# Optimization experiments

Measured on AMD Instinct MI355X. Metric: run time of the kernel, lower is better.

## Reference

```python
import jax, jax.numpy as jnp
import numpy as np

B, FI, FO, K, DIM_STYLE, H, W = 8, 512, 512, 3, 512, 64, 64
EPS = 1e-8


def setup_inputs() -> dict:
    key = jax.random.key(0)
    ks = jax.random.split(key, 5)
    return {
        "x": jax.random.normal(ks[0], (B, FI, H, W), dtype=jnp.float32),
        "style": jax.random.normal(ks[1], (B, DIM_STYLE), dtype=jnp.float32),
        "w": jax.random.normal(ks[2], (FO, FI, K, K), dtype=jnp.float32),
        "mod_w": jax.random.normal(ks[3], (FI, DIM_STYLE), dtype=jnp.float32),
        "mod_b": jax.random.normal(ks[4], (FI,), dtype=jnp.float32),
    }


def _fir_filter(dtype):
    # upfirdn2d.setup_filter([1,3,3,1]): normalize 1D to sum 1, outer product -> 4x4, sum 1
    f1 = jnp.array([1.0, 3.0, 3.0, 1.0], dtype=dtype)
    f1 = f1 / jnp.sum(f1)
    f = jnp.outer(f1, f1)
    # gain = up**2 = 4 applied inside upfirdn2d; filter is symmetric so flip is a no-op
    return (f * 4.0)[::-1, ::-1]


def _mod_conv_up(x, style, w, mod_w, mod_b):
    # modLinear: F.linear(style, mod_w * dim_style**-0.5, bias=mod_b)
    s = style @ (mod_w * (DIM_STYLE ** -0.5)).T + mod_b  # [B, FI]
    # modulate: w_scale * style broadcast over input channels
    w_scale = (FI * K * K) ** -0.5
    wm = w[None] * (w_scale * s[:, None, :, None, None])  # [B, FO, FI, K, K]
    # demodulate
    demod = jax.lax.rsqrt(jnp.sum(wm * wm, axis=(2, 3, 4)) + EPS)  # [B, FO]
    wm = wm * demod[:, :, None, None, None]
    # conv2d_resample up=2 fast path == conv_transpose2d(stride=2, padding=0) per sample,
    def tconv(xs, ws):  # xs [FI,H,W], ws [FO,FI,K,K]
        y = jax.lax.conv_general_dilated(
            xs[None], ws[:, :, ::-1, ::-1],
            window_strides=(1, 1), padding=[(K - 1, K - 1), (K - 1, K - 1)],
            lhs_dilation=(2, 2),
            dimension_numbers=("NCHW", "OIHW", "NCHW"))
        return y[0]

    y = jax.vmap(tconv)(x, wm)  # [B, FO, 2H+1, 2W+1]
    # FIR low-pass: upfirdn2d(pad=[1,1,1,1], gain=4) -> output [B, FO, 2H, 2W]
    f = _fir_filter(y.dtype)
    Bn, C, Hh, Ww = y.shape
    yf = y.reshape(Bn * C, 1, Hh, Ww)
    yf = jax.lax.conv_general_dilated(
        yf, f[None, None], window_strides=(1, 1), padding=[(1, 1), (1, 1)],
        dimension_numbers=("NCHW", "OIHW", "NCHW"))
    return yf.reshape(Bn, C, Hh - 1, Ww - 1)


def reference(x, style, w, mod_w, mod_b):
    return _mod_conv_up(x, style, w, mod_w, mod_b)
```

## Files before the change

kernel.cpp:

```cpp
#include <hip/hip_runtime.h>

typedef _Float16 f16;
typedef f16 f16x8 __attribute__((ext_vector_type(8)));
typedef float f32x4 __attribute__((ext_vector_type(4)));

#define OFF_SMOD  0u
#define OFF_SSQ   16384u
#define OFF_DEMOD 32768u
#define OFF_WSQ   49152u
#define OFF_WPAR  1097728u
#define OFF_XP    5816320u
#define XP_BYTES  35685376u
#define OFF_YP    41501696u
#define WS_NEED   190792704u
#define PLANE     4556

__global__ void style_kernel(const float* __restrict__ style, const float* __restrict__ mod_w,
                             const float* __restrict__ mod_b, float* __restrict__ smod,
                             float* __restrict__ ssq) {
    int b = blockIdx.x;
    int fi = threadIdx.x;
    __shared__ float st[512];
    st[fi] = style[b * 512 + fi];
    __syncthreads();
    float sum = 0.f;
    const float* mw = mod_w + (size_t)fi * 512;
    for (int d = 0; d < 512; ++d) sum += st[d] * mw[d];
    float s = sum * 0.04419417382415922f  + mod_b[fi];
    smod[b * 512 + fi] = s * 0.014731391274719741f ;
    ssq[b * 512 + fi] = s * s;
}

__global__ void wsq_kernel(const float* __restrict__ w, float* __restrict__ wsq) {
    int fo = blockIdx.x;
    int fi = threadIdx.x;
    const float* p = w + ((size_t)fo * 512 + fi) * 9;
    float s = 0.f;
#pragma unroll
    for (int k = 0; k < 9; ++k) { float v = p[k]; s += v * v; }
    wsq[fo * 512 + fi] = s;
}

__global__ void demod_kernel(const float* __restrict__ ssq, const float* __restrict__ wsq,
                             float* __restrict__ demod) {
    int b = blockIdx.x >> 1;
    int fo = (blockIdx.x & 1) * 256 + threadIdx.x;
    __shared__ float sq[512];
    for (int i = threadIdx.x; i < 512; i += 256) sq[i] = ssq[b * 512 + i];
    __syncthreads();
    float sum = 0.f;
    const float* wr = wsq + (size_t)fo * 512;
    for (int fi = 0; fi < 512; ++fi) sum += sq[fi] * wr[fi];
    demod[b * 512 + fo] = rsqrtf(sum * (1.0f / 4608.0f) + 1e-8f);
}

__global__ void xp_kernel(const float* __restrict__ x, const float* __restrict__ smod,
                          f16* __restrict__ xp) {
    int id = blockIdx.x;
    int fc = id & 7;
    int h = (id >> 3) & 63;
    int b = id >> 9;
    int fi0 = fc * 64;
    __shared__ f16 tile[64 * 65];
    int tid = threadIdx.x;
#pragma unroll
    for (int it = 0; it < 16; ++it) {
        int e = it * 256 + tid;
        int i = e >> 6, wc = e & 63;
        float v = x[(((size_t)(b * 512 + fi0 + i)) * 64 + h) * 64 + wc];
        tile[i * 65 + wc] = (f16)(v * smod[b * 512 + fi0 + i]);
    }
    __syncthreads();
#pragma unroll
    for (int it = 0; it < 16; ++it) {
        int e = it * 256 + tid;
        int wc = e >> 6, i = e & 63;
        xp[((size_t)(b * 4356 + (h + 1) * 66 + (wc + 1))) * 512 + fi0 + i] = tile[i * 65 + wc];
    }
}

__global__ void wpar2_kernel(const float* __restrict__ w, f16* __restrict__ wpar2) {
    const int wi_[9] = {8, 6, 2, 0, 7, 1, 5, 3, 4};
    int fo = blockIdx.x;
#pragma unroll
    for (int half = 0; half < 2; ++half) {
        int fi = half * 256 + threadIdx.x;
        const float* p = w + ((size_t)fo * 512 + fi) * 9;
        int fc = fi >> 5, ch = fi & 31;
#pragma unroll
        for (int s = 0; s < 9; ++s)
            wpar2[(((size_t)s * 16 + fc) * 512 + fo) * 32 + ch] = (f16)p[wi_[s]];
    }
}

__global__ void ring2_kernel(f16* __restrict__ P) {
    int idx = blockIdx.x * 256 + threadIdx.x;
    if (idx >= 16384 * 133) return;
    int slab = idx / 133, r = idx - slab * 133;
    f16* base = P + (size_t)slab * PLANE;
    if (r < 68) base[r] = (f16)0.f;
    else base[(r - 67) * 68] = (f16)0.f;
}

template <int C>
__device__ __forceinline__ void tconv_body(const f16* __restrict__ wpar2, const f16* __restrict__ xp,
                                           f16* __restrict__ P, f16* Xs, int b, int fg, int n0t) {
    constexpr int NT   = (C == 0) ? 4 : (C == 3) ? 1 : 2;
    constexpr int SB   = (C == 0) ? 0 : (C == 1) ? 4 : (C == 2) ? 6 : 8;
    constexpr int LB   = (C <= 1) ? 67 : (C == 2) ? 1 : 0;
    constexpr int WOFF = (C <= 1) ? 0 : (C == 2) ? 66 : 67;
    constexpr int WLEN = (C <= 1) ? 195 : (C == 2) ? 129 : 128;
    constexpr int CH4  = WLEN * 4;
    constexpr int offs[4] = {(C == 0) ? -67 : (C == 1) ? -66 : (C == 2) ? -1 : 0,
                             (C == 0) ? -66 : 0, -1, 0};

    int tid = threadIdx.x, lane = tid & 63, wave = tid >> 6;
    int wm = wave >> 1, wn = wave & 1, kb = lane >> 4, lr = lane & 15;
    int n0 = n0t << 7, fo0 = fg << 7;
    int WB = b * 4356 + n0 + WOFF;
    int bmax = b * 4356 + 4356;

    f32x4 acc[4][4];
#pragma unroll
    for (int m = 0; m < 4; ++m)
#pragma unroll
        for (int n = 0; n < 4; ++n) acc[m][n] = (f32x4){0.f, 0.f, 0.f, 0.f};

    int4 xr[4];
    f16x8 afA[4], afB[4];

    const f16* abase = wpar2 + ((size_t)(fo0 + wm * 64 + lr)) * 32 + (size_t)kb * 8;
    auto loadA = [&](int q, f16x8* dst) {
        int fc = q / NT, tap = q - fc * NT;
        const f16* p = abase + (size_t)((SB + tap) * 16 + fc) * (512 * 32);
#pragma unroll
        for (int m = 0; m < 4; ++m) dst[m] = *(const f16x8*)(p + m * 16 * 32);
    };
    auto loadX = [&](int k) {
        int fi0 = k * 32;
#pragma unroll
        for (int it = 0; it < 4; ++it) {
            int idx = it * 256 + tid;
            int4 v = {0, 0, 0, 0};
            if (idx < CH4) {
                int r = idx >> 2, part = idx & 3;
                int pr = WB + r;
                if (pr <= bmax) v = *(const int4*)(xp + ((size_t)pr * 512 + fi0 + part * 8));
            }
            xr[it] = v;
        }
    };
    auto writeX = [&]() {
#pragma unroll
        for (int it = 0; it < 4; ++it) {
            int idx = it * 256 + tid;
            if (idx < CH4) {
                int r = idx >> 2, part = idx & 3;
                *(int4*)((char*)Xs + ((((r * 4 + part) ^ (r & 7)) << 4))) = xr[it];
            }
        }
    };

    loadA(0, afA);
    loadX(0);
    for (int k = 0; k < 16; ++k) {
        __syncthreads();
        writeX();
        __syncthreads();
        if (k < 15) loadX(k + 1);
#pragma unroll
        for (int tap = 0; tap < NT; ++tap) {
            int q = k * NT + tap;
            if (q + 1 < 16 * NT) loadA(q + 1, afB);
            f16x8 bf[4];
#pragma unroll
            for (int n = 0; n < 4; ++n) {
                int r = wn * 64 + n * 16 + lr + offs[tap] + LB;
                bf[n] = *(const f16x8*)((char*)Xs + ((((r * 4 + kb) ^ (r & 7)) << 4)));
            }
            __builtin_amdgcn_s_setprio(1);
#pragma unroll
            for (int m = 0; m < 4; ++m)
#pragma unroll
                for (int n = 0; n < 4; ++n)
                    acc[m][n] = __builtin_amdgcn_mfma_f32_16x16x32_f16(afA[m], bf[n], acc[m][n], 0, 0, 0);
            __builtin_amdgcn_s_setprio(0);
#pragma unroll
            for (int m = 0; m < 4; ++m) afA[m] = afB[m];
        }
    }
    size_t slab = (size_t)(C * 8 + b) * 512;
#pragma unroll
    for (int m = 0; m < 4; ++m) {
#pragma unroll
        for (int j = 0; j < 4; ++j) {
            int fo = fo0 + wm * 64 + m * 16 + kb * 4 + j;
            f16* pb = P + (slab + fo) * PLANE;
#pragma unroll
            for (int n = 0; n < 4; ++n) {
                int nn = n0 + wn * 64 + n * 16 + lr;
                int t = (nn * 993) >> 16;
                int s = nn - t * 66;
                pb[(t + 1) * 68 + (s + 1)] = (f16)acc[m][n][j];
            }
        }
    }
}

__global__ __launch_bounds__(256, 3) void tconv2_kernel(const f16* __restrict__ wpar2,
                                                        const f16* __restrict__ xp,
                                                        f16* __restrict__ P) {
    __shared__ __align__(16) f16 Xs[780 * 8];
    int id = blockIdx.x;
    int b = id & 7;
    int r = id >> 3;
    int c = r / 136;
    int r2 = r - c * 136;
    int fg = r2 / 34;
    int n0t = r2 - fg * 34;
    switch (c) {
        case 0: tconv_body<0>(wpar2, xp, P, Xs, b, fg, n0t); break;
        case 1: tconv_body<1>(wpar2, xp, P, Xs, b, fg, n0t); break;
        case 2: tconv_body<2>(wpar2, xp, P, Xs, b, fg, n0t); break;
        default: tconv_body<3>(wpar2, xp, P, Xs, b, fg, n0t); break;
    }
}

__global__ __launch_bounds__(256) void fir2_kernel(const f16* __restrict__ P,
                                                   const float* __restrict__ demod,
                                                   float* __restrict__ out) {
    int bid = blockIdx.x;
    int rc = bid & 7;
    int fo = (bid >> 3) & 511;
    int b = bid >> 12;
    int OY0 = rc * 16;

    __shared__ f16 yr[19][2][72];
    int tid = threadIdx.x;
#pragma unroll
    for (int it = 0; it < 3; ++it) {
        int ci = it * 256 + tid;
        if (ci < 646) {
            int rr = ci / 34, rem = ci - rr * 34;
            int pxx = rem / 17, ck = rem - pxx * 17;
            int oy = OY0 - 1 + rr;
            int pyy = oy & 1, t = oy >> 1;
            const f16* src = P + ((size_t)((pyy * 2 + pxx) * 8 + b) * 512 + fo) * PLANE
                               + (t + 1) * 68 + ck * 4;
            *(int2*)&yr[rr][pxx][ck * 4] = *(const int2*)src;
        }
    }
    __syncthreads();
    float dm = demod[b * 512 + fo];
    int OX = tid & 127, rg = tid >> 7;
    const float f4[4] = {0.25f, 0.75f, 0.75f, 0.25f};
    float hrow[11];
#pragma unroll
    for (int r = 0; r < 11; ++r) {
        int rr = rg * 8 + r;
        float h = 0.f;
#pragma unroll
        for (int bb = 0; bb < 4; ++bb) {
            int ox = OX - 1 + bb;
            h += f4[bb] * (float)yr[rr][ox & 1][(ox >> 1) + 1];
        }
        hrow[r] = h;
    }
    size_t ob = ((size_t)(b * 512 + fo)) * 128 * 128 + (size_t)OY0 * 128 + OX;
#pragma unroll
    for (int i = 0; i < 8; ++i) {
        float a = f4[0] * hrow[i] + f4[1] * hrow[i + 1] + f4[2] * hrow[i + 2] + f4[3] * hrow[i + 3];
        out[ob + (size_t)(rg * 8 + i) * 128] = a * dm;
    }
}

extern "C" void kernel_launch(void* const* d_in, const int* in_sizes, int n_in,
                              void* d_out, int out_size, void* d_ws, size_t ws_size,
                              hipStream_t stream) {
    const float* x = (const float*)d_in[0];
    const float* style = (const float*)d_in[1];
    const float* w = (const float*)d_in[2];
    const float* mod_w = (const float*)d_in[3];
    const float* mod_b = (const float*)d_in[4];
    float* out = (float*)d_out;

    char* ws = (char*)d_ws;
    float* smod = (float*)(ws + OFF_SMOD);
    float* ssq = (float*)(ws + OFF_SSQ);
    float* demod = (float*)(ws + OFF_DEMOD);
    float* wsq = (float*)(ws + OFF_WSQ);
    f16* wpar2 = (f16*)(ws + OFF_WPAR);
    f16* xp = (f16*)(ws + OFF_XP);
    f16* P = (f16*)(ws + OFF_YP);

    style_kernel<<<8, 512, 0, stream>>>(style, mod_w, mod_b, smod, ssq);
    wsq_kernel<<<512, 512, 0, stream>>>(w, wsq);
    demod_kernel<<<16, 256, 0, stream>>>(ssq, wsq, demod);
    wpar2_kernel<<<512, 256, 0, stream>>>(w, wpar2);
    hipMemsetAsync(xp, 0, XP_BYTES, stream);
    xp_kernel<<<4096, 256, 0, stream>>>(x, smod, xp);
    ring2_kernel<<<8512, 256, 0, stream>>>(P);
    tconv2_kernel<<<4352, 256, 0, stream>>>(wpar2, xp, P);
    fir2_kernel<<<32768, 256, 0, stream>>>(P, demod, out);
}
```

Measured before the change: 401.4 us.

## Double-buffer tconv LDS and register prefetch; load full planes in FIR

The tconv kernel now keeps two LDS buffers for the X tile with a two-deep register prefetch of global X loads, and a triple-buffered A fragment ring. This removes one of the two barriers per k step and overlaps LDS fill with MFMA work. Occupancy drops from 3 to 2 blocks per CU because of the larger LDS footprint and added registers. The FIR kernel is restructured so each block loads all four phase planes of one (b,fo) channel into LDS and runs a rolling vertical filter over 64 rows per thread, which cuts the halo reloads and the block count. PLANE is padded to 4560 so planes stay 16-byte aligned for vector copies.

```diff
diff --git a/kernel.cpp b/kernel.cpp
--- a/kernel.cpp
+++ b/kernel.cpp
@@ -12,8 +12,7 @@
 #define OFF_XP    5816320u
 #define XP_BYTES  35685376u
 #define OFF_YP    41501696u
-#define WS_NEED   190792704u
-#define PLANE     4556
+#define PLANE     4560
 
 __global__ void style_kernel(const float* __restrict__ style, const float* __restrict__ mod_w,
                              const float* __restrict__ mod_b, float* __restrict__ smod,
@@ -111,6 +110,8 @@
     constexpr int WOFF = (C <= 1) ? 0 : (C == 2) ? 66 : 67;
     constexpr int WLEN = (C <= 1) ? 195 : (C == 2) ? 129 : 128;
     constexpr int CH4  = WLEN * 4;
+    constexpr int CH4P = (CH4 + 7) & ~7;
+    constexpr int Q    = 16 * NT;
     constexpr int offs[4] = {(C == 0) ? -67 : (C == 1) ? -66 : (C == 2) ? -1 : 0,
                              (C == 0) ? -66 : 0, -1, 0};
 
@@ -126,8 +127,8 @@
 #pragma unroll
         for (int n = 0; n < 4; ++n) acc[m][n] = (f32x4){0.f, 0.f, 0.f, 0.f};
 
-    int4 xr[4];
-    f16x8 afA[4], afB[4];
+    int4 xr2[2][4];
+    f16x8 afr[3][4], bfr[2][4];
 
     const f16* abase = wpar2 + ((size_t)(fo0 + wm * 64 + lr)) * 32 + (size_t)kb * 8;
     auto loadA = [&](int q, f16x8* dst) {
@@ -136,7 +137,7 @@
 #pragma unroll
         for (int m = 0; m < 4; ++m) dst[m] = *(const f16x8*)(p + m * 16 * 32);
     };
-    auto loadX = [&](int k) {
+    auto loadX = [&](int k, int4* xr) {
         int fi0 = k * 32;
 #pragma unroll
         for (int it = 0; it < 4; ++it) {
@@ -150,45 +151,65 @@
             xr[it] = v;
         }
     };
-    auto writeX = [&]() {
+    auto writeX = [&](int buf, const int4* xr) {
 #pragma unroll
         for (int it = 0; it < 4; ++it) {
             int idx = it * 256 + tid;
             if (idx < CH4) {
                 int r = idx >> 2, part = idx & 3;
-                *(int4*)((char*)Xs + ((((r * 4 + part) ^ (r & 7)) << 4))) = xr[it];
+                *(int4*)((char*)Xs + buf * (CH4P * 16) + (((r * 4 + part) ^ (r & 7)) << 4)) = xr[it];
             }
         }
     };
-
-    loadA(0, afA);
-    loadX(0);
+    auto readBF = [&](int buf, int tap, f16x8* dst) {
+#pragma unroll
+        for (int n = 0; n < 4; ++n) {
+            int r = wn * 64 + n * 16 + lr + offs[tap] + LB;
+            dst[n] = *(const f16x8*)((const char*)Xs + buf * (CH4P * 16) + (((r * 4 + kb) ^ (r & 7)) << 4));
+        }
+    };
+
+    loadX(0, xr2[0]);
+    loadA(0, afr[0]);
+    loadA(1, afr[1 % 3]);
+    writeX(0, xr2[0]);
+    __syncthreads();
+    loadX(1, xr2[1]);
+    readBF(0, 0, bfr[0]);
+
+#pragma unroll
     for (int k = 0; k < 16; ++k) {
-        __syncthreads();
-        writeX();
-        __syncthreads();
-        if (k < 15) loadX(k + 1);
-#pragma unroll
-        for (int tap = 0; tap < NT; ++tap) {
-            int q = k * NT + tap;
-            if (q + 1 < 16 * NT) loadA(q + 1, afB);
-            f16x8 bf[4];
-#pragma unroll
-            for (int n = 0; n < 4; ++n) {
-                int r = wn * 64 + n * 16 + lr + offs[tap] + LB;
-                bf[n] = *(const f16x8*)((char*)Xs + ((((r * 4 + kb) ^ (r & 7)) << 4)));
-            }
+        const int cur = k & 1;
+        if (k < 14) loadX(k + 2, xr2[k & 1]);
+        if (k < 15) writeX(1 - cur, xr2[(k + 1) & 1]);
+#pragma unroll
+        for (int tap = 0; tap < NT - 1; ++tap) {
+            const int q = k * NT + tap;
+            if (q + 2 < Q) loadA(q + 2, afr[(q + 2) % 3]);
+            readBF(cur, tap + 1, bfr[(q + 1) & 1]);
             __builtin_amdgcn_s_setprio(1);
 #pragma unroll
             for (int m = 0; m < 4; ++m)
 #pragma unroll
                 for (int n = 0; n < 4; ++n)
-                    acc[m][n] = __builtin_amdgcn_mfma_f32_16x16x32_f16(afA[m], bf[n], acc[m][n], 0, 0, 0);
+                    acc[m][n] = __builtin_amdgcn_mfma_f32_16x16x32_f16(afr[q % 3][m], bfr[q & 1][n], acc[m][n], 0, 0, 0);
             __builtin_amdgcn_s_setprio(0);
-#pragma unroll
-            for (int m = 0; m < 4; ++m) afA[m] = afB[m];
-        }
-    }
+        }
+        {
+            const int q = k * NT + NT - 1;
+            if (k < 15) __syncthreads();
+            if (q + 2 < Q) loadA(q + 2, afr[(q + 2) % 3]);
+            if (k < 15) readBF(1 - cur, 0, bfr[(q + 1) & 1]);
+            __builtin_amdgcn_s_setprio(1);
+#pragma unroll
+            for (int m = 0; m < 4; ++m)
+#pragma unroll
+                for (int n = 0; n < 4; ++n)
+                    acc[m][n] = __builtin_amdgcn_mfma_f32_16x16x32_f16(afr[q % 3][m], bfr[q & 1][n], acc[m][n], 0, 0, 0);
+            __builtin_amdgcn_s_setprio(0);
+        }
+    }
+
     size_t slab = (size_t)(C * 8 + b) * 512;
 #pragma unroll
     for (int m = 0; m < 4; ++m) {
@@ -207,10 +228,10 @@
     }
 }
 
-__global__ __launch_bounds__(256, 3) void tconv2_kernel(const f16* __restrict__ wpar2,
+__global__ __launch_bounds__(256, 2) void tconv2_kernel(const f16* __restrict__ wpar2,
                                                         const f16* __restrict__ xp,
                                                         f16* __restrict__ P) {
-    __shared__ __align__(16) f16 Xs[780 * 8];
+    __shared__ __align__(16) f16 Xs[2 * 784 * 8];
     int id = blockIdx.x;
     int b = id & 7;
     int r = id >> 3;
@@ -226,51 +247,48 @@
     }
 }
 
-__global__ __launch_bounds__(256) void fir2_kernel(const f16* __restrict__ P,
-                                                   const float* __restrict__ demod,
-                                                   float* __restrict__ out) {
+__global__ __launch_bounds__(256, 4) void fir3_kernel(const f16* __restrict__ P,
+                                                      const float* __restrict__ demod,
+                                                      float* __restrict__ out) {
     int bid = blockIdx.x;
-    int rc = bid & 7;
-    int fo = (bid >> 3) & 511;
-    int b = bid >> 12;
-    int OY0 = rc * 16;
-
-    __shared__ f16 yr[19][2][72];
+    int b = bid & 7, fo = bid >> 3;
+    __shared__ __align__(16) f16 yr[4][4488];
+    const size_t pstep = (size_t)8 * 512 * PLANE;
     int tid = threadIdx.x;
-#pragma unroll
-    for (int it = 0; it < 3; ++it) {
-        int ci = it * 256 + tid;
-        if (ci < 646) {
-            int rr = ci / 34, rem = ci - rr * 34;
-            int pxx = rem / 17, ck = rem - pxx * 17;
-            int oy = OY0 - 1 + rr;
-            int pyy = oy & 1, t = oy >> 1;
-            const f16* src = P + ((size_t)((pyy * 2 + pxx) * 8 + b) * 512 + fo) * PLANE
-                               + (t + 1) * 68 + ck * 4;
-            *(int2*)&yr[rr][pxx][ck * 4] = *(const int2*)src;
+    const f16* src0 = P + ((size_t)(b * 512 + fo)) * PLANE;
+#pragma unroll
+    for (int c = 0; c < 4; ++c) {
+        const int4* src = (const int4*)(src0 + c * pstep);
+        int4* dst = (int4*)(&yr[c][0]);
+#pragma unroll
+        for (int it = 0; it < 3; ++it) {
+            int idx = it * 256 + tid;
+            if (idx < 561) dst[idx] = src[idx];
         }
     }
     __syncthreads();
     float dm = demod[b * 512 + fo];
     int OX = tid & 127, rg = tid >> 7;
-    const float f4[4] = {0.25f, 0.75f, 0.75f, 0.25f};
-    float hrow[11];
-#pragma unroll
-    for (int r = 0; r < 11; ++r) {
-        int rr = rg * 8 + r;
-        float h = 0.f;
-#pragma unroll
-        for (int bb = 0; bb < 4; ++bb) {
-            int ox = OX - 1 + bb;
-            h += f4[bb] * (float)yr[rr][ox & 1][(ox >> 1) + 1];
-        }
-        hrow[r] = h;
-    }
-    size_t ob = ((size_t)(b * 512 + fo)) * 128 * 128 + (size_t)OY0 * 128 + OX;
-#pragma unroll
-    for (int i = 0; i < 8; ++i) {
-        float a = f4[0] * hrow[i] + f4[1] * hrow[i + 1] + f4[2] * hrow[i + 2] + f4[3] * hrow[i + 3];
-        out[ob + (size_t)(rg * 8 + i) * 128] = a * dm;
+    int OYb = rg * 64;
+    int e = OX & 1;
+    int c0o = (1 - e) * 4488 + (((OX - 1) >> 1) + 1);
+    int c1o = e * 4488 + ((OX >> 1) + 1);
+    int c2o = (1 - e) * 4488 + (((OX + 1) >> 1) + 1);
+    int c3o = e * 4488 + (((OX + 2) >> 1) + 1);
+    const f16* yf = &yr[0][0];
+    size_t obase = ((size_t)(b * 512 + fo)) * 16384 + OX;
+    float h0 = 0.f, h1 = 0.f, h2 = 0.f, h3 = 0.f;
+#pragma unroll 4
+    for (int i = 0; i < 67; ++i) {
+        int oy = OYb - 1 + i;
+        int base = (oy & 1) * (2 * 4488) + ((oy >> 1) + 1) * 68;
+        float h = 0.25f * ((float)yf[base + c0o] + (float)yf[base + c3o])
+                + 0.75f * ((float)yf[base + c1o] + (float)yf[base + c2o]);
+        h0 = h1; h1 = h2; h2 = h3; h3 = h;
+        if (i >= 3) {
+            float a = 0.25f * (h0 + h3) + 0.75f * (h1 + h2);
+            out[obase + (size_t)(OYb + i - 3) * 128] = a * dm;
+        }
     }
 }
 
@@ -301,5 +319,5 @@
     xp_kernel<<<4096, 256, 0, stream>>>(x, smod, xp);
     ring2_kernel<<<8512, 256, 0, stream>>>(P);
     tconv2_kernel<<<4352, 256, 0, stream>>>(wpar2, xp, P);
-    fir2_kernel<<<32768, 256, 0, stream>>>(P, demod, out);
-}
+    fir3_kernel<<<4096, 256, 0, stream>>>(P, demod, out);
+}
```

Result: slower. 423.8 us (+5.6%).
